# Performance work log

Hardware: AMD Instinct MI355X
Metric: run time of the kernel (lower is better)

The kernel has to match this reference:

```python
import jax, jax.numpy as jnp
import numpy as np

NEG_SLOPE = 0.2
N, E, NNZ, IN, H, C = 100000, 50000, 800000, 128, 8, 16


def setup_inputs() -> dict:
    key = jax.random.key(0)
    ks = jax.random.split(key, 8)
    X = jax.random.normal(ks[0], (N, IN), jnp.float32)
    W_typed = jax.random.normal(ks[1], (4, IN, H * C), jnp.float32) * (1.0 / np.sqrt(IN))
    att_e = jax.random.normal(ks[2], (4, H, C), jnp.float32) * 0.1
    att_v = jax.random.normal(ks[3], (4, H, C), jnp.float32) * 0.1
    vertex = jax.random.randint(ks[4], (NNZ,), 0, N, jnp.int32)
    edges = jax.random.randint(ks[5], (NNZ,), 0, E, jnp.int32)
    vtype = jax.random.randint(ks[6], (N,), 0, 4, jnp.int32)
    etype = jax.random.randint(ks[7], (E,), 0, 4, jnp.int32)
    return {"X": X, "W_typed": W_typed, "att_e": att_e, "att_v": att_v,
            "vertex": vertex, "edges": edges, "vtype": vtype, "etype": etype}


def _segment_softmax(logits, seg, num):
    # numerically-stable softmax over segments (PyG-style, eps in denominator)
    m = jax.ops.segment_max(logits, seg, num_segments=num)
    ex = jnp.exp(logits - m[seg])
    s = jax.ops.segment_sum(ex, seg, num_segments=num)
    return ex / (s[seg] + 1e-16)


def reference(X, W_typed, att_e, att_v, vertex, edges, vtype, etype):
    # typed linear: project with all 4 type weights, select per node type
    Xall = jnp.einsum('ni,tio->tno', X, W_typed)        # [4, N, H*C]
    X0 = Xall[vtype, jnp.arange(N)]                     # [N, H*C]
    Xn = X0.reshape(N, H, C)
    Xve = Xn[vertex]                                    # [NNZ, H, C] gather vertex->incidence
    # vertex->edge attention, typed by edge type of each incidence
    beta = jnp.sum(Xve * att_e[etype[edges]], axis=-1)  # [NNZ, H]
    beta = jax.nn.leaky_relu(beta, NEG_SLOPE)
    beta = _segment_softmax(beta, edges, E)
    Xe = jax.nn.relu(jax.ops.segment_sum(Xve * beta[..., None], edges, num_segments=E))  # [E, H, C]
    Xe = Xe[edges]                                      # [NNZ, H, C] gather edge->incidence
    # edge->vertex attention, typed by node type of each incidence's vertex
    alpha = jnp.sum(Xe * att_v[vtype[vertex]], axis=-1)  # [NNZ, H]
    alpha = jax.nn.leaky_relu(alpha, NEG_SLOPE)
    alpha = _segment_softmax(alpha, vertex, N)
    Xv = jax.ops.segment_sum(Xe * alpha[..., None], vertex, num_segments=N)  # [N, H, C]
    return Xv.reshape(N, H * C)
```

## Files before the change

### kernel.cpp

```cpp
#include <hip/hip_runtime.h>

typedef __attribute__((ext_vector_type(8))) short bf16x8;
typedef __attribute__((ext_vector_type(4))) float f32x4;

#define NEG_SLOPE 0.2f

__device__ __forceinline__ unsigned short f2bf(float f){
  unsigned u = __float_as_uint(f);
  u = (u + 0x7fffu + ((u >> 16) & 1u)) >> 16;
  return (unsigned short)u;
}
__device__ __forceinline__ float bflo(unsigned u){ return __uint_as_float(u << 16); }
__device__ __forceinline__ float bfhi(unsigned u){ return __uint_as_float(u & 0xffff0000u); }
__device__ __forceinline__ float lrelu(float x){ return x > 0.f ? x : NEG_SLOPE * x; }

__global__ __launch_bounds__(256) void k_prep(
    const int* __restrict__ vtype, int N, int* __restrict__ tcnt, int nbHN,
    const float* __restrict__ W, short* __restrict__ Bfrag){
  __shared__ int lcnt[4];
  int b = (int)blockIdx.x;
  if (b < nbHN){
    if (threadIdx.x < 4) lcnt[threadIdx.x] = 0;
    __syncthreads();
    int i = b * 256 + threadIdx.x;
    if (i < N) atomicAdd(&lcnt[vtype[i]], 1);
    __syncthreads();
    if (threadIdx.x < 4 && lcnt[threadIdx.x] > 0)
      atomicAdd(tcnt + threadIdx.x, lcnt[threadIdx.x]);
    return;
  }
  b -= nbHN;
  int u = b * 256 + threadIdx.x;
  int j = u & 7, lane = (u >> 3) & 63, ct = (u >> 9) & 31, ks = u >> 14;
  int k = ks * 32 + ((lane >> 4) << 3) + j;
  int col = (ct << 4) + (lane & 15);
  int t = col >> 7, o = col & 127;
  Bfrag[u] = (short)f2bf(W[(t * 128 + k) * 128 + o]);
}

__global__ __launch_bounds__(256) void k_nodeplace(
    const int* __restrict__ vtype, int N, const int* __restrict__ tcnt,
    int* __restrict__ tcur, int* __restrict__ nsorted){
  __shared__ int lcnt[4];
  __shared__ int gbase[4];
  __shared__ int spb[4];
  int t = threadIdx.x;
  if (t < 4) lcnt[t] = 0;
  if (t == 0){
    int run = 0;
    #pragma unroll
    for (int k = 0; k < 4; ++k){ spb[k] = run; run += ((tcnt[k] + 63) >> 6) << 6; }
  }
  __syncthreads();
  int i = (int)blockIdx.x * 256 + t;
  int tt = 0, rank = 0;
  bool valid = i < N;
  if (valid){ tt = vtype[i]; rank = atomicAdd(&lcnt[tt], 1); }
  __syncthreads();
  if (t < 4 && lcnt[t] > 0) gbase[t] = atomicAdd(tcur + t, lcnt[t]);
  __syncthreads();
  if (valid) nsorted[spb[tt] + gbase[tt] + rank] = i;
}

__global__ __launch_bounds__(256, 3) void k_gemm_hist(const float* __restrict__ X,
    const short* __restrict__ Bfrag, const int* __restrict__ nsorted,
    const int* __restrict__ tcnt, unsigned short* __restrict__ X0,
    const int* __restrict__ edges, const int* __restrict__ vertex, int NNZ,
    int* __restrict__ cnt, int E,
    int* __restrict__ rank_e, int* __restrict__ rank_v, int nbHist){
  __shared__ short shB[8 * 4 * 64 * 8];
  const int tid = threadIdx.x;
  const int q = (int)blockIdx.x / 3, r = (int)blockIdx.x % 3;

  if (r != 0){
    int hb = 2 * q + (r - 1);
    if (hb < nbHist){
      int i = hb * 256 + tid;
      if (i < NNZ){
        rank_e[i] = atomicAdd(cnt + edges[i], 1);
        rank_v[i] = atomicAdd(cnt + E + vertex[i], 1);
      }
    }
    return;
  }

  const int rowIdx = q * 64;
  int pb1, pb2, pb3;
  {
    int run = ((tcnt[0] + 63) >> 6) << 6; pb1 = run;
    run    += ((tcnt[1] + 63) >> 6) << 6; pb2 = run;
    run    += ((tcnt[2] + 63) >> 6) << 6; pb3 = run;
  }
  const int t = (rowIdx >= pb1) + (rowIdx >= pb2) + (rowIdx >= pb3);

  const bf16x8* Bv = (const bf16x8*)Bfrag;
  bf16x8* shBv = (bf16x8*)shB;
  #pragma unroll
  for (int v = 0; v < 8; ++v){
    int item = v * 256 + tid;
    int slab = item >> 6, ln = item & 63;
    int ks = slab >> 3, ctl = slab & 7;
    shBv[item] = Bv[((ks * 32 + 8 * t + ctl) * 64) + ln];
  }

  const int w = tid >> 6, lane = tid & 63;
  const int m = lane & 15, qq = lane >> 4;
  const int node = nsorted[rowIdx + w * 16 + m];

  bf16x8 afrag[4];
  #pragma unroll
  for (int ks = 0; ks < 4; ++ks){
    bf16x8 f;
    if (node >= 0){
      const float4* src = (const float4*)(X + (size_t)node * 128 + ks * 32 + qq * 8);
      float4 a = src[0], b = src[1];
      f[0]=(short)f2bf(a.x); f[1]=(short)f2bf(a.y); f[2]=(short)f2bf(a.z); f[3]=(short)f2bf(a.w);
      f[4]=(short)f2bf(b.x); f[5]=(short)f2bf(b.y); f[6]=(short)f2bf(b.z); f[7]=(short)f2bf(b.w);
    } else {
      #pragma unroll
      for (int z = 0; z < 8; ++z) f[z] = 0;
    }
    afrag[ks] = f;
  }

  f32x4 acc[8];
  #pragma unroll
  for (int ct = 0; ct < 8; ++ct){
    acc[ct][0]=0.f; acc[ct][1]=0.f; acc[ct][2]=0.f; acc[ct][3]=0.f;
  }

  __syncthreads();
  #pragma unroll
  for (int ctl = 0; ctl < 8; ++ctl){
    #pragma unroll
    for (int ks = 0; ks < 4; ++ks){
      bf16x8 bf = shBv[(ks * 8 + ctl) * 64 + lane];
      acc[ctl] = __builtin_amdgcn_mfma_f32_16x16x32_bf16(afrag[ks], bf, acc[ctl], 0, 0, 0);
    }
  }

  const int col0 = lane & 15;
  #pragma unroll
  for (int rr = 0; rr < 4; ++rr){
    int row = nsorted[rowIdx + w * 16 + qq * 4 + rr];
    if (row < 0) continue;
    #pragma unroll
    for (int ctl = 0; ctl < 8; ++ctl)
      X0[(size_t)row * 128 + ctl * 16 + col0] = f2bf(acc[ctl][rr]);
  }
}

__global__ __launch_bounds__(256) void k_scanA(const int* __restrict__ cnt, int S,
                                               int* __restrict__ bsum){
  __shared__ int sh[256];
  int base = blockIdx.x * 1024 + threadIdx.x * 4;
  int s = 0;
  #pragma unroll
  for (int k = 0; k < 4; ++k){ int idx = base + k; if (idx < S) s += cnt[idx]; }
  sh[threadIdx.x] = s; __syncthreads();
  for (int off = 128; off > 0; off >>= 1){
    if (threadIdx.x < off) sh[threadIdx.x] += sh[threadIdx.x + off];
    __syncthreads();
  }
  if (threadIdx.x == 0) bsum[blockIdx.x] = sh[0];
}

__global__ __launch_bounds__(256) void k_scanC3(const int* __restrict__ cnt, int S,
    const int* __restrict__ bsum, int nb, int* __restrict__ offs){
  __shared__ int shb[256];
  __shared__ int sh[256];
  int t = threadIdx.x;
  int b = (int)blockIdx.x;
  shb[t] = (t < nb) ? bsum[t] : 0;
  __syncthreads();
  for (int off = 1; off < 256; off <<= 1){
    int v = (t >= off) ? shb[t - off] : 0; __syncthreads();
    shb[t] += v; __syncthreads();
  }
  int bbase = (b == 0) ? 0 : shb[b - 1];
  int base = b * 1024 + t * 4;
  int c[4]; int s = 0;
  #pragma unroll
  for (int k = 0; k < 4; ++k){ int idx = base + k; c[k] = (idx < S) ? cnt[idx] : 0; s += c[k]; }
  sh[t] = s; __syncthreads();
  for (int off = 1; off < 256; off <<= 1){
    int v = (t >= off) ? sh[t - off] : 0; __syncthreads();
    sh[t] += v; __syncthreads();
  }
  int run = bbase + sh[t] - s;
  #pragma unroll
  for (int k = 0; k < 4; ++k){
    int idx = base + k;
    if (idx < S){ offs[idx] = run; run += c[k]; }
  }
}

__global__ __launch_bounds__(256) void k_place_e(
    const int* __restrict__ edges, const int* __restrict__ vertex, int NNZ,
    const int* __restrict__ offs, const int* __restrict__ rank_e,
    int* __restrict__ rows){
  int i = (int)blockIdx.x * 256 + (int)threadIdx.x;
  if (i < NNZ) rows[offs[edges[i]] + rank_e[i]] = vertex[i];
}

template<int OUT_BF16>
__device__ __forceinline__ void seg_body(const uint4* __restrict__ feat,
    const float* __restrict__ att, const int* __restrict__ rows_sorted,
    const int* __restrict__ offs, const int* __restrict__ cnt,
    const int* __restrict__ stype, void* __restrict__ outbuf,
    int S, int blockId, int tid){
  int wid = tid >> 6, lane = tid & 63;
  int s = blockId * 4 + wid;
  if (s >= S) return;
  int t = stype[s];
  int sub = lane >> 4, lane16 = lane & 15;
  const float4* ap = (const float4*)(att + t * 128 + lane16 * 8);
  float4 A0 = ap[0], A1 = ap[1];
  int start = offs[s], len = cnt[s];
  float denom = 0.f;
  float acc[8];
  #pragma unroll
  for (int e = 0; e < 8; ++e) acc[e] = 0.f;

  for (int base = 0; base < len; base += 64){
    int m = len - base; if (m > 64) m = 64;
    int idx = 0;
    if (lane < m) idx = rows_sorted[start + base + lane];
    int ng = (m + 3) >> 2;
    uint4 uA = make_uint4(0,0,0,0), uB = make_uint4(0,0,0,0);
    {
      int r0 = __shfl(idx, sub);
      if (sub < m) uA = feat[(size_t)r0 * 16 + lane16];
      int r1 = __shfl(idx, 4 + sub);
      if (4 + sub < m) uB = feat[(size_t)r1 * 16 + lane16];
    }
    for (int g = 0; g < ng; g += 2){
      {
        uint4 u = uA;
        int nr = (g + 2) * 4 + sub;
        int rn = __shfl(idx, nr & 63);
        if (nr < m) uA = feat[(size_t)rn * 16 + lane16];
        float x0 = bflo(u.x), x1 = bfhi(u.x), x2 = bflo(u.y), x3 = bfhi(u.y);
        float x4 = bflo(u.z), x5 = bfhi(u.z), x6 = bflo(u.w), x7 = bfhi(u.w);
        float p = x0*A0.x + x1*A0.y + x2*A0.z + x3*A0.w
                + x4*A1.x + x5*A1.y + x6*A1.z + x7*A1.w;
        p += __shfl_xor(p, 1);
        float wgt = __expf(lrelu(p));
        wgt = (g * 4 + sub < m) ? wgt : 0.f;
        denom += wgt;
        acc[0] += wgt*x0; acc[1] += wgt*x1; acc[2] += wgt*x2; acc[3] += wgt*x3;
        acc[4] += wgt*x4; acc[5] += wgt*x5; acc[6] += wgt*x6; acc[7] += wgt*x7;
      }
      if (g + 1 < ng){
        uint4 u = uB;
        int nr = (g + 3) * 4 + sub;
        int rn = __shfl(idx, nr & 63);
        if (nr < m) uB = feat[(size_t)rn * 16 + lane16];
        float x0 = bflo(u.x), x1 = bfhi(u.x), x2 = bflo(u.y), x3 = bfhi(u.y);
        float x4 = bflo(u.z), x5 = bfhi(u.z), x6 = bflo(u.w), x7 = bfhi(u.w);
        float p = x0*A0.x + x1*A0.y + x2*A0.z + x3*A0.w
                + x4*A1.x + x5*A1.y + x6*A1.z + x7*A1.w;
        p += __shfl_xor(p, 1);
        float wgt = __expf(lrelu(p));
        wgt = ((g + 1) * 4 + sub < m) ? wgt : 0.f;
        denom += wgt;
        acc[0] += wgt*x0; acc[1] += wgt*x1; acc[2] += wgt*x2; acc[3] += wgt*x3;
        acc[4] += wgt*x4; acc[5] += wgt*x5; acc[6] += wgt*x6; acc[7] += wgt*x7;
      }
    }
  }
  denom += __shfl_xor(denom, 16);
  denom += __shfl_xor(denom, 32);
  #pragma unroll
  for (int e = 0; e < 8; ++e){
    acc[e] += __shfl_xor(acc[e], 16);
    acc[e] += __shfl_xor(acc[e], 32);
  }
  float inv = 1.f / (denom + 1e-16f);
  float v[8];
  #pragma unroll
  for (int e = 0; e < 8; ++e) v[e] = acc[e] * inv;

  if constexpr (OUT_BF16){
    if (sub == 0){
      uint4 pw;
      pw.x = (unsigned)f2bf(fmaxf(v[0],0.f)) | ((unsigned)f2bf(fmaxf(v[1],0.f)) << 16);
      pw.y = (unsigned)f2bf(fmaxf(v[2],0.f)) | ((unsigned)f2bf(fmaxf(v[3],0.f)) << 16);
      pw.z = (unsigned)f2bf(fmaxf(v[4],0.f)) | ((unsigned)f2bf(fmaxf(v[5],0.f)) << 16);
      pw.w = (unsigned)f2bf(fmaxf(v[6],0.f)) | ((unsigned)f2bf(fmaxf(v[7],0.f)) << 16);
      ((uint4*)outbuf)[(size_t)s * 16 + lane16] = pw;
    }
  } else {
    if (sub == 0){
      float4* op = (float4*)outbuf;
      op[(size_t)s * 32 + lane16 * 2]     = make_float4(v[0], v[1], v[2], v[3]);
      op[(size_t)s * 32 + lane16 * 2 + 1] = make_float4(v[4], v[5], v[6], v[7]);
    }
  }
}

__global__ __launch_bounds__(256) void k_seg1_pv(
    const int* __restrict__ edges, const int* __restrict__ vertex, int NNZ,
    const int* __restrict__ offs, const int* __restrict__ rank_v,
    int* __restrict__ rows, int E, int nbPlace,
    const uint4* __restrict__ X0, const float* __restrict__ att_e,
    const int* __restrict__ cnt, const int* __restrict__ etype,
    void* __restrict__ Xe, int nbSeg){
  const int q = (int)blockIdx.x / 5, r = (int)blockIdx.x % 5;
  if (r == 0){
    if (q < nbPlace){
      int i = q * 256 + (int)threadIdx.x;
      if (i < NNZ) rows[offs[E + vertex[i]] + rank_v[i]] = edges[i];
    }
    return;
  }
  int segBlk = q * 4 + (r - 1);
  if (segBlk >= nbSeg) return;
  seg_body<1>(X0, att_e, rows, offs, cnt, etype, Xe, E, segBlk, threadIdx.x);
}

__global__ __launch_bounds__(256) void k_seg2(const uint4* __restrict__ Xe,
    const float* __restrict__ att_v, const int* __restrict__ rows,
    const int* __restrict__ offs, const int* __restrict__ cnt,
    const int* __restrict__ vtype, float* __restrict__ out, int N){
  seg_body<0>(Xe, att_v, rows, offs, cnt, vtype, out, N,
              (int)blockIdx.x, threadIdx.x);
}

extern "C" void kernel_launch(void* const* d_in, const int* in_sizes, int n_in,
                              void* d_out, int out_size, void* d_ws, size_t ws_size,
                              hipStream_t stream){
  const float* X      = (const float*)d_in[0];
  const float* W      = (const float*)d_in[1];
  const float* att_e  = (const float*)d_in[2];
  const float* att_v  = (const float*)d_in[3];
  const int*   vertex = (const int*)d_in[4];
  const int*   edges  = (const int*)d_in[5];
  const int*   vtype  = (const int*)d_in[6];
  const int*   etype  = (const int*)d_in[7];
  float* out = (float*)d_out;
  const int N   = in_sizes[0] / 128;
  const int NNZ = in_sizes[4];
  const int E   = in_sizes[7];
  const int S   = E + N;

  const int nbI = (NNZ + 255) / 256;
  const int nbHN = (N + 255) / 256;
  const int nbS = (S + 1023) / 1024;
  const int nbSeg1 = (E + 3) / 4;
  const int nbPad = (N + 252 + 63) / 64;
  const int nsortedCap = nbPad * 64;
  const int nQA = (nbPad > (nbI + 1) / 2) ? nbPad : (nbI + 1) / 2;
  const int nQB = (nbI > (nbSeg1 + 3) / 4) ? nbI : (nbSeg1 + 3) / 4;

  char* wp = (char*)d_ws;
  int* cnt    = (int*)wp; wp += (size_t)S * 4;
  int* tcnt   = (int*)wp; wp += 16;
  int* tcur   = (int*)wp; wp += 16;
  int* offs   = (int*)wp; wp += (size_t)S * 4;
  int* bsum   = (int*)wp; wp += 1024;
  int* rows   = (int*)wp; wp += (size_t)2 * NNZ * 4;
  int* nsorted= (int*)wp; wp += (size_t)nsortedCap * 4;
  int* rank_e = (int*)wp; wp += (size_t)NNZ * 4;
  int* rank_v = (int*)wp; wp += (size_t)NNZ * 4;
  unsigned short* X0 = (unsigned short*)wp; wp += (size_t)N * 128 * 2;
  unsigned short* Xe = (unsigned short*)wp; wp += (size_t)E * 128 * 2;
  short* Bfrag = (short*)wp; wp += (size_t)65536 * 2;

  hipMemsetAsync(cnt, 0, (size_t)(S + 8) * 4, stream);
  hipMemsetAsync(nsorted, 0xFF, (size_t)nsortedCap * 4, stream);

  k_prep<<<nbHN + 256, 256, 0, stream>>>(vtype, N, tcnt, nbHN, W, Bfrag);
  k_nodeplace<<<nbHN, 256, 0, stream>>>(vtype, N, tcnt, tcur, nsorted);

  k_gemm_hist<<<3 * nQA, 256, 0, stream>>>(X, Bfrag, nsorted, tcnt,
      (unsigned short*)X0, edges, vertex, NNZ, cnt, E, rank_e, rank_v, nbI);

  k_scanA<<<nbS, 256, 0, stream>>>(cnt, S, bsum);
  k_scanC3<<<nbS, 256, 0, stream>>>(cnt, S, bsum, nbS, offs);
  k_place_e<<<nbI, 256, 0, stream>>>(edges, vertex, NNZ, offs, rank_e, rows);

  k_seg1_pv<<<5 * nQB, 256, 0, stream>>>(edges, vertex, NNZ, offs, rank_v,
      rows, E, nbI, (const uint4*)X0, att_e, cnt, etype, Xe, nbSeg1);

  k_seg2<<<(N + 3) / 4, 256, 0, stream>>>((const uint4*)Xe, att_v,
      rows, offs + E, cnt + E, vtype, out, N);
}
```

Baseline: 304.7 us.

## Replace global-atomic incidence histogram with range-partitioned LDS histograms

The per-incidence rank/count pass moves from global atomics into 32 dedicated blocks, 16 for edges and 16 for vertices. Each block owns a key range held as a histogram in shared memory, scans every key, and writes ranks and final counts for its range. This is meant to remove contended global atomic traffic during the GEMM kernel. The cost is that every histogram block reads the whole key array, so a few long-running blocks may stretch the kernel's tail.

```diff
diff --git a/kernel.cpp b/kernel.cpp
--- a/kernel.cpp
+++ b/kernel.cpp
@@ -62,28 +62,51 @@
   if (valid) nsorted[spb[tt] + gbase[tt] + rank] = i;
 }
 
+#define NB_H 16
+
 __global__ __launch_bounds__(256, 3) void k_gemm_hist(const float* __restrict__ X,
     const short* __restrict__ Bfrag, const int* __restrict__ nsorted,
     const int* __restrict__ tcnt, unsigned short* __restrict__ X0,
     const int* __restrict__ edges, const int* __restrict__ vertex, int NNZ,
-    int* __restrict__ cnt, int E,
-    int* __restrict__ rank_e, int* __restrict__ rank_v, int nbHist){
+    int* __restrict__ cnt, int E, int N,
+    int* __restrict__ rank_e, int* __restrict__ rank_v){
   __shared__ short shB[8 * 4 * 64 * 8];
   const int tid = threadIdx.x;
-  const int q = (int)blockIdx.x / 3, r = (int)blockIdx.x % 3;
-
-  if (r != 0){
-    int hb = 2 * q + (r - 1);
-    if (hb < nbHist){
-      int i = hb * 256 + tid;
-      if (i < NNZ){
-        rank_e[i] = atomicAdd(cnt + edges[i], 1);
-        rank_v[i] = atomicAdd(cnt + E + vertex[i], 1);
-      }
-    }
+  const int b = (int)blockIdx.x;
+
+  if (b < 2 * NB_H){
+    const int isV = (b >= NB_H) ? 1 : 0;
+    const int bb = isV ? (b - NB_H) : b;
+    const int K = isV ? N : E;
+    const int R = (K + NB_H - 1) / NB_H;
+    const int lo = bb * R;
+    const int hi = (lo + R < K) ? (lo + R) : K;
+    const int* __restrict__ keys = isV ? vertex : edges;
+    int* __restrict__ rnk = isV ? rank_v : rank_e;
+    int* __restrict__ cp  = cnt + (isV ? E : 0);
+    int* h = (int*)shB;
+    for (int k = tid; k < R; k += 256) h[k] = 0;
+    __syncthreads();
+    const int4* k4 = (const int4*)keys;
+    int nv = NNZ >> 2;
+    for (int j = tid; j < nv; j += 256){
+      int4 kk = k4[j];
+      int i = j << 2;
+      if (kk.x >= lo && kk.x < hi) rnk[i]     = atomicAdd(&h[kk.x - lo], 1);
+      if (kk.y >= lo && kk.y < hi) rnk[i + 1] = atomicAdd(&h[kk.y - lo], 1);
+      if (kk.z >= lo && kk.z < hi) rnk[i + 2] = atomicAdd(&h[kk.z - lo], 1);
+      if (kk.w >= lo && kk.w < hi) rnk[i + 3] = atomicAdd(&h[kk.w - lo], 1);
+    }
+    for (int i = (nv << 2) + tid; i < NNZ; i += 256){
+      int kk = keys[i];
+      if (kk >= lo && kk < hi) rnk[i] = atomicAdd(&h[kk - lo], 1);
+    }
+    __syncthreads();
+    for (int k = tid; lo + k < hi; k += 256) cp[lo + k] = h[k];
     return;
   }
 
+  const int q = b - 2 * NB_H;
   const int rowIdx = q * 64;
   int pb1, pb2, pb3;
   {
@@ -113,9 +136,9 @@
     bf16x8 f;
     if (node >= 0){
       const float4* src = (const float4*)(X + (size_t)node * 128 + ks * 32 + qq * 8);
-      float4 a = src[0], b = src[1];
+      float4 a = src[0], bq = src[1];
       f[0]=(short)f2bf(a.x); f[1]=(short)f2bf(a.y); f[2]=(short)f2bf(a.z); f[3]=(short)f2bf(a.w);
-      f[4]=(short)f2bf(b.x); f[5]=(short)f2bf(b.y); f[6]=(short)f2bf(b.z); f[7]=(short)f2bf(b.w);
+      f[4]=(short)f2bf(bq.x); f[5]=(short)f2bf(bq.y); f[6]=(short)f2bf(bq.z); f[7]=(short)f2bf(bq.w);
     } else {
       #pragma unroll
       for (int z = 0; z < 8; ++z) f[z] = 0;
@@ -350,7 +373,6 @@
   const int nbSeg1 = (E + 3) / 4;
   const int nbPad = (N + 252 + 63) / 64;
   const int nsortedCap = nbPad * 64;
-  const int nQA = (nbPad > (nbI + 1) / 2) ? nbPad : (nbI + 1) / 2;
   const int nQB = (nbI > (nbSeg1 + 3) / 4) ? nbI : (nbSeg1 + 3) / 4;
 
   char* wp = (char*)d_ws;
@@ -373,8 +395,8 @@
   k_prep<<<nbHN + 256, 256, 0, stream>>>(vtype, N, tcnt, nbHN, W, Bfrag);
   k_nodeplace<<<nbHN, 256, 0, stream>>>(vtype, N, tcnt, tcur, nsorted);
 
-  k_gemm_hist<<<3 * nQA, 256, 0, stream>>>(X, Bfrag, nsorted, tcnt,
-      (unsigned short*)X0, edges, vertex, NNZ, cnt, E, rank_e, rank_v, nbI);
+  k_gemm_hist<<<2 * NB_H + nbPad, 256, 0, stream>>>(X, Bfrag, nsorted, tcnt,
+      (unsigned short*)X0, edges, vertex, NNZ, cnt, E, N, rank_e, rank_v);
 
   k_scanA<<<nbS, 256, 0, stream>>>(cnt, S, bsum);
   k_scanC3<<<nbS, 256, 0, stream>>>(cnt, S, bsum, nbS, offs);
```

Measured after the change: 720.3 us. 136% more time.

## Precompute per-row attention weights for all four types before segment passes

Applied to the files above, without the earlier changes.

The attention weights exp(leaky_relu(x·att_t)) depend only on the source row and the segment type. The GEMM kernel now computes them for all four edge types per node into a bf16 table We, and the seg1 kernel computes the four vertex-type weights per edge into Wv. The segment loops then load one precomputed weight per row instead of recomputing a dot product, a shuffle and an exp for every incidence. This adds extra writes and an extra small gather per incidence, rounds the weights to bf16, and reuses the rank_e buffer as storage for Wv.

```diff
diff --git a/kernel.cpp b/kernel.cpp
--- a/kernel.cpp
+++ b/kernel.cpp
@@ -67,8 +67,10 @@
     const int* __restrict__ tcnt, unsigned short* __restrict__ X0,
     const int* __restrict__ edges, const int* __restrict__ vertex, int NNZ,
     int* __restrict__ cnt, int E,
-    int* __restrict__ rank_e, int* __restrict__ rank_v, int nbHist){
-  __shared__ short shB[8 * 4 * 64 * 8];
+    int* __restrict__ rank_e, int* __restrict__ rank_v, int nbHist,
+    const float* __restrict__ att_e, unsigned short* __restrict__ We){
+  __shared__ __align__(16) short shB[16896];
+  __shared__ __align__(16) float shAtt[512];
   const int tid = threadIdx.x;
   const int q = (int)blockIdx.x / 3, r = (int)blockIdx.x % 3;
 
@@ -93,6 +95,9 @@
   }
   const int t = (rowIdx >= pb1) + (rowIdx >= pb2) + (rowIdx >= pb3);
 
+  shAtt[tid] = att_e[tid];
+  shAtt[tid + 256] = att_e[tid + 256];
+
   const bf16x8* Bv = (const bf16x8*)Bfrag;
   bf16x8* shBv = (bf16x8*)shB;
   #pragma unroll
@@ -113,9 +118,9 @@
     bf16x8 f;
     if (node >= 0){
       const float4* src = (const float4*)(X + (size_t)node * 128 + ks * 32 + qq * 8);
-      float4 a = src[0], b = src[1];
+      float4 a = src[0], bq = src[1];
       f[0]=(short)f2bf(a.x); f[1]=(short)f2bf(a.y); f[2]=(short)f2bf(a.z); f[3]=(short)f2bf(a.w);
-      f[4]=(short)f2bf(b.x); f[5]=(short)f2bf(b.y); f[6]=(short)f2bf(b.z); f[7]=(short)f2bf(b.w);
+      f[4]=(short)f2bf(bq.x); f[5]=(short)f2bf(bq.y); f[6]=(short)f2bf(bq.z); f[7]=(short)f2bf(bq.w);
     } else {
       #pragma unroll
       for (int z = 0; z < 8; ++z) f[z] = 0;
@@ -147,6 +152,38 @@
     #pragma unroll
     for (int ctl = 0; ctl < 8; ++ctl)
       X0[(size_t)row * 128 + ctl * 16 + col0] = f2bf(acc[ctl][rr]);
+  }
+
+  __syncthreads();
+  float* shF = (float*)shB;
+  #pragma unroll
+  for (int ctl = 0; ctl < 8; ++ctl){
+    #pragma unroll
+    for (int rr = 0; rr < 4; ++rr)
+      shF[(w * 16 + qq * 4 + rr) * 132 + ctl * 16 + col0] = acc[ctl][rr];
+  }
+  __syncthreads();
+  const int prow = tid >> 2, part = tid & 3;
+  const int pnode = nsorted[rowIdx + prow];
+  if (pnode >= 0){
+    const float4* xr = (const float4*)(shF + prow * 132 + part * 32);
+    float4 xv[8];
+    #pragma unroll
+    for (int i = 0; i < 8; ++i) xv[i] = xr[i];
+    #pragma unroll
+    for (int tt = 0; tt < 4; ++tt){
+      const float4* ae = (const float4*)(shAtt + tt * 128 + part * 32);
+      float s0 = 0.f, s1 = 0.f;
+      #pragma unroll
+      for (int i = 0; i < 4; ++i){
+        float4 a = ae[i], b = ae[4 + i];
+        s0 += xv[i].x*a.x + xv[i].y*a.y + xv[i].z*a.z + xv[i].w*a.w;
+        s1 += xv[4+i].x*b.x + xv[4+i].y*b.y + xv[4+i].z*b.z + xv[4+i].w*b.w;
+      }
+      float w0 = __expf(lrelu(s0)), w1 = __expf(lrelu(s1));
+      ((unsigned*)We)[(size_t)pnode * 16 + tt * 4 + part] =
+          (unsigned)f2bf(w0) | ((unsigned)f2bf(w1) << 16);
+    }
   }
 }
 
@@ -205,17 +242,17 @@
 
 template<int OUT_BF16>
 __device__ __forceinline__ void seg_body(const uint4* __restrict__ feat,
-    const float* __restrict__ att, const int* __restrict__ rows_sorted,
+    const unsigned short* __restrict__ wgt, const int* __restrict__ rows_sorted,
     const int* __restrict__ offs, const int* __restrict__ cnt,
     const int* __restrict__ stype, void* __restrict__ outbuf,
-    int S, int blockId, int tid){
+    int S, int blockId, int tid,
+    const float* __restrict__ att_next, unsigned short* __restrict__ wnext){
   int wid = tid >> 6, lane = tid & 63;
   int s = blockId * 4 + wid;
   if (s >= S) return;
   int t = stype[s];
   int sub = lane >> 4, lane16 = lane & 15;
-  const float4* ap = (const float4*)(att + t * 128 + lane16 * 8);
-  float4 A0 = ap[0], A1 = ap[1];
+  int toff = t * 8 + (lane16 >> 1);
   int start = offs[s], len = cnt[s];
   float denom = 0.f;
   float acc[8];
@@ -228,44 +265,41 @@
     if (lane < m) idx = rows_sorted[start + base + lane];
     int ng = (m + 3) >> 2;
     uint4 uA = make_uint4(0,0,0,0), uB = make_uint4(0,0,0,0);
+    float wA = 0.f, wB = 0.f;
     {
       int r0 = __shfl(idx, sub);
-      if (sub < m) uA = feat[(size_t)r0 * 16 + lane16];
+      if (sub < m){ uA = feat[(size_t)r0 * 16 + lane16];
+                    wA = bflo((unsigned)wgt[(size_t)r0 * 32 + toff]); }
       int r1 = __shfl(idx, 4 + sub);
-      if (4 + sub < m) uB = feat[(size_t)r1 * 16 + lane16];
+      if (4 + sub < m){ uB = feat[(size_t)r1 * 16 + lane16];
+                        wB = bflo((unsigned)wgt[(size_t)r1 * 32 + toff]); }
     }
     for (int g = 0; g < ng; g += 2){
       {
-        uint4 u = uA;
+        uint4 u = uA; float w = wA;
         int nr = (g + 2) * 4 + sub;
         int rn = __shfl(idx, nr & 63);
-        if (nr < m) uA = feat[(size_t)rn * 16 + lane16];
-        float x0 = bflo(u.x), x1 = bfhi(u.x), x2 = bflo(u.y), x3 = bfhi(u.y);
-        float x4 = bflo(u.z), x5 = bfhi(u.z), x6 = bflo(u.w), x7 = bfhi(u.w);
-        float p = x0*A0.x + x1*A0.y + x2*A0.z + x3*A0.w
-                + x4*A1.x + x5*A1.y + x6*A1.z + x7*A1.w;
-        p += __shfl_xor(p, 1);
-        float wgt = __expf(lrelu(p));
-        wgt = (g * 4 + sub < m) ? wgt : 0.f;
-        denom += wgt;
-        acc[0] += wgt*x0; acc[1] += wgt*x1; acc[2] += wgt*x2; acc[3] += wgt*x3;
-        acc[4] += wgt*x4; acc[5] += wgt*x5; acc[6] += wgt*x6; acc[7] += wgt*x7;
+        if (nr < m){ uA = feat[(size_t)rn * 16 + lane16];
+                     wA = bflo((unsigned)wgt[(size_t)rn * 32 + toff]); }
+        else wA = 0.f;
+        denom += w;
+        acc[0] += w * bflo(u.x); acc[1] += w * bfhi(u.x);
+        acc[2] += w * bflo(u.y); acc[3] += w * bfhi(u.y);
+        acc[4] += w * bflo(u.z); acc[5] += w * bfhi(u.z);
+        acc[6] += w * bflo(u.w); acc[7] += w * bfhi(u.w);
       }
       if (g + 1 < ng){
-        uint4 u = uB;
+        uint4 u = uB; float w = wB;
         int nr = (g + 3) * 4 + sub;
         int rn = __shfl(idx, nr & 63);
-        if (nr < m) uB = feat[(size_t)rn * 16 + lane16];
-        float x0 = bflo(u.x), x1 = bfhi(u.x), x2 = bflo(u.y), x3 = bfhi(u.y);
-        float x4 = bflo(u.z), x5 = bfhi(u.z), x6 = bflo(u.w), x7 = bfhi(u.w);
-        float p = x0*A0.x + x1*A0.y + x2*A0.z + x3*A0.w
-                + x4*A1.x + x5*A1.y + x6*A1.z + x7*A1.w;
-        p += __shfl_xor(p, 1);
-        float wgt = __expf(lrelu(p));
-        wgt = ((g + 1) * 4 + sub < m) ? wgt : 0.f;
-        denom += wgt;
-        acc[0] += wgt*x0; acc[1] += wgt*x1; acc[2] += wgt*x2; acc[3] += wgt*x3;
-        acc[4] += wgt*x4; acc[5] += wgt*x5; acc[6] += wgt*x6; acc[7] += wgt*x7;
+        if (nr < m){ uB = feat[(size_t)rn * 16 + lane16];
+                     wB = bflo((unsigned)wgt[(size_t)rn * 32 + toff]); }
+        else wB = 0.f;
+        denom += w;
+        acc[0] += w * bflo(u.x); acc[1] += w * bfhi(u.x);
+        acc[2] += w * bflo(u.y); acc[3] += w * bfhi(u.y);
+        acc[4] += w * bflo(u.z); acc[5] += w * bfhi(u.z);
+        acc[6] += w * bflo(u.w); acc[7] += w * bfhi(u.w);
       }
     }
   }
@@ -282,12 +316,24 @@
   for (int e = 0; e < 8; ++e) v[e] = acc[e] * inv;
 
   if constexpr (OUT_BF16){
+    #pragma unroll
+    for (int e = 0; e < 8; ++e) v[e] = fmaxf(v[e], 0.f);
+    #pragma unroll
+    for (int tt = 0; tt < 4; ++tt){
+      const float* av = att_next + tt * 128 + lane16 * 8;
+      float p = v[0]*av[0] + v[1]*av[1] + v[2]*av[2] + v[3]*av[3]
+              + v[4]*av[4] + v[5]*av[5] + v[6]*av[6] + v[7]*av[7];
+      p += __shfl_xor(p, 1);
+      float wv = __expf(lrelu(p));
+      if (sub == 0 && (lane16 & 1) == 0)
+        wnext[(size_t)s * 32 + tt * 8 + (lane16 >> 1)] = f2bf(wv);
+    }
     if (sub == 0){
       uint4 pw;
-      pw.x = (unsigned)f2bf(fmaxf(v[0],0.f)) | ((unsigned)f2bf(fmaxf(v[1],0.f)) << 16);
-      pw.y = (unsigned)f2bf(fmaxf(v[2],0.f)) | ((unsigned)f2bf(fmaxf(v[3],0.f)) << 16);
-      pw.z = (unsigned)f2bf(fmaxf(v[4],0.f)) | ((unsigned)f2bf(fmaxf(v[5],0.f)) << 16);
-      pw.w = (unsigned)f2bf(fmaxf(v[6],0.f)) | ((unsigned)f2bf(fmaxf(v[7],0.f)) << 16);
+      pw.x = (unsigned)f2bf(v[0]) | ((unsigned)f2bf(v[1]) << 16);
+      pw.y = (unsigned)f2bf(v[2]) | ((unsigned)f2bf(v[3]) << 16);
+      pw.z = (unsigned)f2bf(v[4]) | ((unsigned)f2bf(v[5]) << 16);
+      pw.w = (unsigned)f2bf(v[6]) | ((unsigned)f2bf(v[7]) << 16);
       ((uint4*)outbuf)[(size_t)s * 16 + lane16] = pw;
     }
   } else {
@@ -303,9 +349,10 @@
     const int* __restrict__ edges, const int* __restrict__ vertex, int NNZ,
     const int* __restrict__ offs, const int* __restrict__ rank_v,
     int* __restrict__ rows, int E, int nbPlace,
-    const uint4* __restrict__ X0, const float* __restrict__ att_e,
+    const uint4* __restrict__ X0, const unsigned short* __restrict__ We,
     const int* __restrict__ cnt, const int* __restrict__ etype,
-    void* __restrict__ Xe, int nbSeg){
+    void* __restrict__ Xe, int nbSeg,
+    const float* __restrict__ att_v, unsigned short* __restrict__ Wv){
   const int q = (int)blockIdx.x / 5, r = (int)blockIdx.x % 5;
   if (r == 0){
     if (q < nbPlace){
@@ -316,15 +363,16 @@
   }
   int segBlk = q * 4 + (r - 1);
   if (segBlk >= nbSeg) return;
-  seg_body<1>(X0, att_e, rows, offs, cnt, etype, Xe, E, segBlk, threadIdx.x);
+  seg_body<1>(X0, We, rows, offs, cnt, etype, Xe, E, segBlk, threadIdx.x,
+              att_v, Wv);
 }
 
 __global__ __launch_bounds__(256) void k_seg2(const uint4* __restrict__ Xe,
-    const float* __restrict__ att_v, const int* __restrict__ rows,
+    const unsigned short* __restrict__ Wv, const int* __restrict__ rows,
     const int* __restrict__ offs, const int* __restrict__ cnt,
     const int* __restrict__ vtype, float* __restrict__ out, int N){
-  seg_body<0>(Xe, att_v, rows, offs, cnt, vtype, out, N,
-              (int)blockIdx.x, threadIdx.x);
+  seg_body<0>(Xe, Wv, rows, offs, cnt, vtype, out, N,
+              (int)blockIdx.x, threadIdx.x, nullptr, nullptr);
 }
 
 extern "C" void kernel_launch(void* const* d_in, const int* in_sizes, int n_in,
@@ -366,6 +414,8 @@
   unsigned short* X0 = (unsigned short*)wp; wp += (size_t)N * 128 * 2;
   unsigned short* Xe = (unsigned short*)wp; wp += (size_t)E * 128 * 2;
   short* Bfrag = (short*)wp; wp += (size_t)65536 * 2;
+  unsigned short* We = (unsigned short*)wp; wp += (size_t)N * 32 * 2;
+  unsigned short* Wv = (unsigned short*)rank_e;
 
   hipMemsetAsync(cnt, 0, (size_t)(S + 8) * 4, stream);
   hipMemsetAsync(nsorted, 0xFF, (size_t)nsortedCap * 4, stream);
@@ -374,15 +424,16 @@
   k_nodeplace<<<nbHN, 256, 0, stream>>>(vtype, N, tcnt, tcur, nsorted);
 
   k_gemm_hist<<<3 * nQA, 256, 0, stream>>>(X, Bfrag, nsorted, tcnt,
-      (unsigned short*)X0, edges, vertex, NNZ, cnt, E, rank_e, rank_v, nbI);
+      (unsigned short*)X0, edges, vertex, NNZ, cnt, E, rank_e, rank_v, nbI,
+      att_e, We);
 
   k_scanA<<<nbS, 256, 0, stream>>>(cnt, S, bsum);
   k_scanC3<<<nbS, 256, 0, stream>>>(cnt, S, bsum, nbS, offs);
   k_place_e<<<nbI, 256, 0, stream>>>(edges, vertex, NNZ, offs, rank_e, rows);
 
   k_seg1_pv<<<5 * nQB, 256, 0, stream>>>(edges, vertex, NNZ, offs, rank_v,
-      rows, E, nbI, (const uint4*)X0, att_e, cnt, etype, Xe, nbSeg1);
-
-  k_seg2<<<(N + 3) / 4, 256, 0, stream>>>((const uint4*)Xe, att_v,
+      rows, E, nbI, (const uint4*)X0, We, cnt, etype, Xe, nbSeg1, att_v, Wv);
+
+  k_seg2<<<(N + 3) / 4, 256, 0, stream>>>((const uint4*)Xe, Wv,
       rows, offs + E, cnt + E, vtype, out, N);
 }
```

Result: slower. 328.8 us (+7.9%).

## Split CSR build into edge and vertex phases, overlapping vertex histogram with seg1

Applied to the files above, without the earlier changes.

The vertex-side histogram moves out of the GEMM kernel and into the seg1 kernel, where its blocks are interleaved with the edge-segment softmax work. The scan is split into separate edge and vertex scans, and a separate vertex placement kernel writes into the second half of rows. The aim is to shorten the critical path before seg1 and spread the atomic traffic more evenly. The cost is three extra kernel launches and a longer serial chain between seg1 and seg2.

```diff
diff --git a/kernel.cpp b/kernel.cpp
--- a/kernel.cpp
+++ b/kernel.cpp
@@ -65,9 +65,8 @@
 __global__ __launch_bounds__(256, 3) void k_gemm_hist(const float* __restrict__ X,
     const short* __restrict__ Bfrag, const int* __restrict__ nsorted,
     const int* __restrict__ tcnt, unsigned short* __restrict__ X0,
-    const int* __restrict__ edges, const int* __restrict__ vertex, int NNZ,
-    int* __restrict__ cnt, int E,
-    int* __restrict__ rank_e, int* __restrict__ rank_v, int nbHist){
+    const int* __restrict__ edges, int NNZ,
+    int* __restrict__ cnt, int* __restrict__ rank_e, int nbHist){
   __shared__ short shB[8 * 4 * 64 * 8];
   const int tid = threadIdx.x;
   const int q = (int)blockIdx.x / 3, r = (int)blockIdx.x % 3;
@@ -76,10 +75,7 @@
     int hb = 2 * q + (r - 1);
     if (hb < nbHist){
       int i = hb * 256 + tid;
-      if (i < NNZ){
-        rank_e[i] = atomicAdd(cnt + edges[i], 1);
-        rank_v[i] = atomicAdd(cnt + E + vertex[i], 1);
-      }
+      if (i < NNZ) rank_e[i] = atomicAdd(cnt + edges[i], 1);
     }
     return;
   }
@@ -113,9 +109,9 @@
     bf16x8 f;
     if (node >= 0){
       const float4* src = (const float4*)(X + (size_t)node * 128 + ks * 32 + qq * 8);
-      float4 a = src[0], b = src[1];
+      float4 a = src[0], bq = src[1];
       f[0]=(short)f2bf(a.x); f[1]=(short)f2bf(a.y); f[2]=(short)f2bf(a.z); f[3]=(short)f2bf(a.w);
-      f[4]=(short)f2bf(b.x); f[5]=(short)f2bf(b.y); f[6]=(short)f2bf(b.z); f[7]=(short)f2bf(b.w);
+      f[4]=(short)f2bf(bq.x); f[5]=(short)f2bf(bq.y); f[6]=(short)f2bf(bq.z); f[7]=(short)f2bf(bq.w);
     } else {
       #pragma unroll
       for (int z = 0; z < 8; ++z) f[z] = 0;
@@ -201,6 +197,14 @@
     int* __restrict__ rows){
   int i = (int)blockIdx.x * 256 + (int)threadIdx.x;
   if (i < NNZ) rows[offs[edges[i]] + rank_e[i]] = vertex[i];
+}
+
+__global__ __launch_bounds__(256) void k_place_v(
+    const int* __restrict__ edges, const int* __restrict__ vertex, int NNZ,
+    const int* __restrict__ offsV, const int* __restrict__ rank_v,
+    int* __restrict__ rowsV){
+  int i = (int)blockIdx.x * 256 + (int)threadIdx.x;
+  if (i < NNZ) rowsV[offsV[vertex[i]] + rank_v[i]] = edges[i];
 }
 
 template<int OUT_BF16>
@@ -299,18 +303,18 @@
   }
 }
 
-__global__ __launch_bounds__(256) void k_seg1_pv(
-    const int* __restrict__ edges, const int* __restrict__ vertex, int NNZ,
-    const int* __restrict__ offs, const int* __restrict__ rank_v,
-    int* __restrict__ rows, int E, int nbPlace,
+__global__ __launch_bounds__(256) void k_seg1_histv(
+    const int* __restrict__ vertex, int NNZ,
+    int* __restrict__ cntV, int* __restrict__ rank_v, int nbHist,
     const uint4* __restrict__ X0, const float* __restrict__ att_e,
+    const int* __restrict__ rows, const int* __restrict__ offs,
     const int* __restrict__ cnt, const int* __restrict__ etype,
-    void* __restrict__ Xe, int nbSeg){
+    void* __restrict__ Xe, int E, int nbSeg){
   const int q = (int)blockIdx.x / 5, r = (int)blockIdx.x % 5;
   if (r == 0){
-    if (q < nbPlace){
+    if (q < nbHist){
       int i = q * 256 + (int)threadIdx.x;
-      if (i < NNZ) rows[offs[E + vertex[i]] + rank_v[i]] = edges[i];
+      if (i < NNZ) rank_v[i] = atomicAdd(cntV + vertex[i], 1);
     }
     return;
   }
@@ -346,7 +350,8 @@
 
   const int nbI = (NNZ + 255) / 256;
   const int nbHN = (N + 255) / 256;
-  const int nbS = (S + 1023) / 1024;
+  const int nbSE = (E + 1023) / 1024;
+  const int nbSV = (N + 1023) / 1024;
   const int nbSeg1 = (E + 3) / 4;
   const int nbPad = (N + 252 + 63) / 64;
   const int nsortedCap = nbPad * 64;
@@ -374,15 +379,20 @@
   k_nodeplace<<<nbHN, 256, 0, stream>>>(vtype, N, tcnt, tcur, nsorted);
 
   k_gemm_hist<<<3 * nQA, 256, 0, stream>>>(X, Bfrag, nsorted, tcnt,
-      (unsigned short*)X0, edges, vertex, NNZ, cnt, E, rank_e, rank_v, nbI);
-
-  k_scanA<<<nbS, 256, 0, stream>>>(cnt, S, bsum);
-  k_scanC3<<<nbS, 256, 0, stream>>>(cnt, S, bsum, nbS, offs);
+      (unsigned short*)X0, edges, NNZ, cnt, rank_e, nbI);
+
+  k_scanA<<<nbSE, 256, 0, stream>>>(cnt, E, bsum);
+  k_scanC3<<<nbSE, 256, 0, stream>>>(cnt, E, bsum, nbSE, offs);
   k_place_e<<<nbI, 256, 0, stream>>>(edges, vertex, NNZ, offs, rank_e, rows);
 
-  k_seg1_pv<<<5 * nQB, 256, 0, stream>>>(edges, vertex, NNZ, offs, rank_v,
-      rows, E, nbI, (const uint4*)X0, att_e, cnt, etype, Xe, nbSeg1);
+  k_seg1_histv<<<5 * nQB, 256, 0, stream>>>(vertex, NNZ, cnt + E, rank_v, nbI,
+      (const uint4*)X0, att_e, rows, offs, cnt, etype, Xe, E, nbSeg1);
+
+  k_scanA<<<nbSV, 256, 0, stream>>>(cnt + E, N, bsum);
+  k_scanC3<<<nbSV, 256, 0, stream>>>(cnt + E, N, bsum, nbSV, offs + E);
+  k_place_v<<<nbI, 256, 0, stream>>>(edges, vertex, NNZ, offs + E, rank_v,
+      rows + NNZ);
 
   k_seg2<<<(N + 3) / 4, 256, 0, stream>>>((const uint4*)Xe, att_v,
-      rows, offs + E, cnt + E, vtype, out, N);
-}
+      rows + NNZ, offs + E, cnt + E, vtype, out, N);
+}
```

Result: no change. 302.2 us (-0.8%).
